# Kernel optimization log

Hardware: AMD Instinct MI355X
Metric: run time of the kernel (lower is better)

The kernel has to match this reference:

```python
import jax, jax.numpy as jnp
import numpy as np


def setup_inputs() -> dict:
    key = jax.random.key(0)
    kq, kk, kv = jax.random.split(key, 3)
    B, H, QL, KL, D = 2, 32, 512, 4096, 128
    return {
        "Q": jax.random.normal(kq, (B, H, QL, D), dtype=jnp.float32),
        "K": jax.random.normal(kk, (B, H, KL, D), dtype=jnp.float32),
        "V": jax.random.normal(kv, (B, H, KL, D), dtype=jnp.float32),
        "proj_dim": 32,
    }


def reference(Q, K, V, proj_dim):
    bsz, num_heads, q_len, head_dim = Q.shape
    kv_len = K.shape[2]
    bh = bsz * num_heads

    # ---- prepare(K, V): SVD of centered K, low-rank basis B ----
    K_r = K.reshape(bh, kv_len, head_dim)
    V_r = V.reshape(bh, kv_len, head_dim)
    K_centered = (K_r - K_r.mean(axis=1, keepdims=True)).astype(jnp.float32)
    _, _, Vh = jnp.linalg.svd(K_centered, full_matrices=False)  # [bh, d, d]
    Bmat = jnp.swapaxes(Vh[:, :proj_dim, :], -2, -1).astype(K.dtype)  # [bh, d, r]
    K_proj = jnp.matmul(K_r, Bmat)  # [bh, kv_len, r]

    # ---- forward(Q): project Q, full score matrix, softmax, weighted V ----
    Q_r = Q.reshape(bh, q_len, head_dim)
    Q_proj = jnp.matmul(Q_r, Bmat)  # [bh, q_len, r]
    scale = 1.0 / (proj_dim ** 0.5)
    scores = jnp.matmul(Q_proj, jnp.swapaxes(K_proj, 1, 2)) * scale  # [bh, q_len, kv_len]
    weights = jax.nn.softmax(scores, axis=-1)
    out = jnp.matmul(weights, V_r)  # [bh, q_len, d]
    return out.reshape(bsz, num_heads, q_len, head_dim)
```

## Files before the change

kernel.cpp:

```cpp
#include <hip/hip_runtime.h>

#define BH 64
#define KLEN 4096
#define QLEN 512
#define DIM 128
#define RP 32
#define NSWEEP 6

__global__ __launch_bounds__(256) void gram_kernel(const float* __restrict__ K,
                                                   float* __restrict__ Gpart,
                                                   float* __restrict__ Spart) {
    int bh = blockIdx.y, chunk = blockIdx.x;
    const float* Kb = K + ((size_t)bh * KLEN + (size_t)chunk * 1024) * DIM;
    __shared__ float Kt[32][129];
    int t = threadIdx.x;
    int ty = t >> 4, tx = t & 15;
    float acc[8][8];
#pragma unroll
    for (int i = 0; i < 8; i++)
#pragma unroll
        for (int j = 0; j < 8; j++) acc[i][j] = 0.f;
    float s_acc = 0.f;
    for (int tile = 0; tile < 32; tile++) {
        __syncthreads();
        for (int k = 0; k < 16; k++) {
            int idx = t + k * 256;
            Kt[idx >> 7][idx & 127] = Kb[tile * 32 * DIM + idx];
        }
        __syncthreads();
#pragma unroll 4
        for (int r = 0; r < 32; r++) {
            float a_[8], b_[8];
#pragma unroll
            for (int i = 0; i < 8; i++) a_[i] = Kt[r][ty * 8 + i];
#pragma unroll
            for (int j = 0; j < 8; j++) b_[j] = Kt[r][tx * 8 + j];
#pragma unroll
            for (int i = 0; i < 8; i++)
#pragma unroll
                for (int j = 0; j < 8; j++) acc[i][j] += a_[i] * b_[j];
        }
        if (t < 128) { float ss = 0.f; for (int r = 0; r < 32; r++) ss += Kt[r][t]; s_acc += ss; }
    }
    float* Gb = Gpart + ((size_t)chunk * BH + bh) * DIM * DIM;
#pragma unroll
    for (int i = 0; i < 8; i++)
#pragma unroll
        for (int j = 0; j < 8; j++) Gb[(ty * 8 + i) * DIM + tx * 8 + j] = acc[i][j];
    if (t < 128) Spart[((size_t)chunk * BH + bh) * DIM + t] = s_acc;
}

__device__ __forceinline__ void pair_pq(int r, int x, int& p, int& q) {
    if (x == 0) { p = 127; q = r; }
    else {
        int a = r + x;       a -= (a >= 127) ? 127 : 0;
        int b = r + 127 - x; b -= (b >= 127) ? 127 : 0;
        p = a; q = b;
    }
}

__global__ __launch_bounds__(1024) void jacobi_kernel(const float* __restrict__ Gpart,
                                                      const float* __restrict__ Spart,
                                                      float* __restrict__ Bout) {
    __shared__ float C[128][129];
    __shared__ float Vm[32][129];
    __shared__ float2 csA[2][64];
    __shared__ float diag[128];
    int slice = blockIdx.x, bh = blockIdx.y, t = threadIdx.x;
    const size_t gslab = (size_t)BH * DIM * DIM;
    const float* Gb = Gpart + (size_t)bh * DIM * DIM;

#define CGET(a, b) C[min(a, b)][max(a, b)]

    if (t < 128) {
        float s = 0.f;
#pragma unroll
        for (int c = 0; c < 4; c++) s += Spart[((size_t)c * BH + bh) * DIM + t];
        diag[t] = s;
    }
    __syncthreads();
    for (int k = 0; k < 16; k++) {
        int idx = t + k * 1024;
        int i = idx >> 7, j = idx & 127;
        if (i <= j) {
            float g = Gb[idx] + Gb[gslab + idx] + Gb[2 * gslab + idx] + Gb[3 * gslab + idx];
            C[i][j] = g - diag[i] * diag[j] * (1.0f / 4096.0f);
        }
    }
    for (int k = 0; k < 4; k++) {
        int idx = t + k * 1024;
        int kk = idx >> 7, j = idx & 127;
        Vm[kk][j] = (32 * slice + kk == j) ? 1.0f : 0.0f;
    }
    __syncthreads();
    if (t < 64) {
        int p, q;
        pair_pq(0, t, p, q);
        float app = C[min(p, p)][p], aqq = C[q][q], apq = CGET(p, q);
        float c = 1.0f, s = 0.0f;
        if (apq != 0.0f) {
            float tau = (aqq - app) / (2.0f * apq);
            float root = sqrtf(1.0f + tau * tau);
            float tt = (tau >= 0.0f) ? 1.0f / (tau + root) : 1.0f / (tau - root);
            c = 1.0f / sqrtf(1.0f + tt * tt);
            s = tt * c;
        }
        csA[0][t] = make_float2(c, s);
    }
    __syncthreads();

    int ti0, tj0, ti1, tj1, ti2 = 0, tj2 = 0;
    {
        auto unrank = [](int task, int& i, int& j) {
            if (task < 64) { i = task; j = task; return; }
            int L = task - 64, ii = 0;
            while (L >= 63 - ii) { L -= 63 - ii; ii++; }
            i = ii; j = ii + 1 + L;
        };
        unrank(t, ti0, tj0);
        unrank(t + 1024, ti1, tj1);
        if (t < 32) unrank(t + 2048, ti2, tj2);
    }

    const int NR = NSWEEP * 127;
    int r = 0;
    for (int sr = 0; sr < NR; sr++) {
        int cur = sr & 1, nxt = cur ^ 1;
        {
            auto task = [&](int i, int j) {
                int pi, qi; pair_pq(r, i, pi, qi);
                float2 csi = csA[cur][i];
                if (i == j) {
                    float app = C[min(pi, qi)][min(pi, qi)];
                    float aqq = C[max(pi, qi)][max(pi, qi)];
                    app = C[pi][pi]; aqq = C[qi][qi];
                    float apq = CGET(pi, qi);
                    float a1 = csi.x * app - csi.y * apq, b1 = csi.y * app + csi.x * apq;
                    float d1 = csi.x * apq - csi.y * aqq, e1 = csi.y * apq + csi.x * aqq;
                    C[pi][pi] = csi.x * a1 - csi.y * d1;
                    CGET(pi, qi) = csi.x * b1 - csi.y * e1;
                    C[qi][qi] = csi.y * b1 + csi.x * e1;
                } else {
                    int pj, qj; pair_pq(r, j, pj, qj);
                    float2 csj = csA[cur][j];
                    float a = CGET(pi, pj), b = CGET(pi, qj), d = CGET(qi, pj), e = CGET(qi, qj);
                    float a1 = csj.x * a - csj.y * b, b1 = csj.y * a + csj.x * b;
                    float d1 = csj.x * d - csj.y * e, e1 = csj.y * d + csj.x * e;
                    CGET(pi, pj) = csi.x * a1 - csi.y * d1;
                    CGET(qi, pj) = csi.y * a1 + csi.x * d1;
                    CGET(pi, qj) = csi.x * b1 - csi.y * e1;
                    CGET(qi, qj) = csi.y * b1 + csi.x * e1;
                }
            };
            task(ti0, tj0);
            task(ti1, tj1);
            if (t < 32) task(ti2, tj2);
        }
        __syncthreads();
        if (t < 64) {
            if (sr + 1 < NR) {
                int r2 = (r + 1 == 127) ? 0 : r + 1;
                int p, q;
                pair_pq(r2, t, p, q);
                float app = C[p][p], aqq = C[q][q], apq = CGET(p, q);
                float c = 1.0f, s = 0.0f;
                if (apq != 0.0f) {
                    float tau = (aqq - app) / (2.0f * apq);
                    float root = sqrtf(1.0f + tau * tau);
                    float tt = (tau >= 0.0f) ? 1.0f / (tau + root) : 1.0f / (tau - root);
                    c = 1.0f / sqrtf(1.0f + tt * tt);
                    s = tt * c;
                }
                csA[nxt][t] = make_float2(c, s);
            }
        } else {
            int tt = t - 64;
            for (int tau = tt; tau < 2048; tau += 960) {
                int x = tau & 63, k = tau >> 6;
                int pj, qj; pair_pq(r, x, pj, qj);
                float2 cs = csA[cur][x];
                float u = Vm[k][pj], v = Vm[k][qj];
                Vm[k][pj] = cs.x * u - cs.y * v;
                Vm[k][qj] = cs.y * u + cs.x * v;
            }
        }
        __syncthreads();
        r = (r + 1 == 127) ? 0 : r + 1;
    }

    if (t < 128) diag[t] = C[t][t];
    __syncthreads();
    if (t < 128) {
        float dt = diag[t];
        int rank = 0;
        for (int j = 0; j < 128; j++) {
            float dj = diag[j];
            rank += (dj > dt) || (dj == dt && j < t);
        }
        if (rank < RP) {
            float* Bb = Bout + (size_t)bh * DIM * RP;
            for (int k = 0; k < 32; k++) Bb[(size_t)(32 * slice + k) * RP + rank] = Vm[k][t];
        }
    }
#undef CGET
}

__global__ __launch_bounds__(256) void proj_kernel(const float* __restrict__ X,
                                                   const float* __restrict__ Bmat,
                                                   float* __restrict__ Y, int nrows) {
    int bh = blockIdx.y, rb = blockIdx.x;
    __shared__ float Bl[128][33];
    __shared__ float Xt[64][129];
    int t = threadIdx.x;
    for (int k = 0; k < 16; k++) {
        int idx = t + k * 256;
        Bl[idx >> 5][idx & 31] = Bmat[(size_t)bh * DIM * RP + idx];
    }
    const float* Xb = X + ((size_t)bh * nrows + (size_t)rb * 64) * DIM;
    for (int k = 0; k < 32; k++) {
        int idx = t + k * 256;
        Xt[idx >> 7][idx & 127] = Xb[idx];
    }
    __syncthreads();
    int row = t >> 2, rg = (t & 3) * 8;
    float acc[8] = {0.f, 0.f, 0.f, 0.f, 0.f, 0.f, 0.f, 0.f};
    for (int k = 0; k < 128; k++) {
        float xv = Xt[row][k];
#pragma unroll
        for (int rr = 0; rr < 8; rr++) acc[rr] += xv * Bl[k][rg + rr];
    }
    float* Yb = Y + ((size_t)bh * nrows + (size_t)rb * 64) * RP + row * RP + rg;
#pragma unroll
    for (int rr = 0; rr < 8; rr++) Yb[rr] = acc[rr];
}

__global__ __launch_bounds__(256, 2) void attn_kernel(const float* __restrict__ Qp,
                                                      const float* __restrict__ Kp,
                                                      const float* __restrict__ Vg,
                                                      float* __restrict__ Out) {
    const float SCALE = 0.1767766953f;
    int qt = blockIdx.x, bh = blockIdx.y;
    __shared__ float Kpl[128][36];
    __shared__ float Vt[32][132];
    __shared__ float Sl[64][132];
    int t = threadIdx.x;
    int q = t >> 2, g = t & 3;
    float qreg[32];
    const float* Qb = Qp + ((size_t)bh * QLEN + (size_t)qt * 64 + q) * RP;
#pragma unroll
    for (int r = 0; r < 32; r++) qreg[r] = Qb[r];
    float acc[32];
#pragma unroll
    for (int i = 0; i < 32; i++) acc[i] = 0.f;
    float m_run = -INFINITY, l_run = 0.0f;

    for (int kt = 0; kt < 32; kt++) {
        __syncthreads();
        const float4* Kpb = (const float4*)(Kp + ((size_t)bh * KLEN + (size_t)kt * 128) * RP);
        for (int k = 0; k < 4; k++) {
            int idx4 = t + k * 256;
            int j = idx4 >> 3, r4 = idx4 & 7;
            *(float4*)&Kpl[j][r4 * 4] = Kpb[idx4];
        }
        __syncthreads();
        float sreg[32];
#pragma unroll
        for (int jj = 0; jj < 32; jj++) {
            int j = jj * 4 + g;
            float s = 0.f;
#pragma unroll
            for (int r4 = 0; r4 < 8; r4++) {
                float4 kv = *(const float4*)&Kpl[j][r4 * 4];
                s += qreg[r4 * 4 + 0] * kv.x + qreg[r4 * 4 + 1] * kv.y
                   + qreg[r4 * 4 + 2] * kv.z + qreg[r4 * 4 + 3] * kv.w;
            }
            sreg[jj] = s * SCALE;
        }
        float mx = sreg[0];
#pragma unroll
        for (int jj = 1; jj < 32; jj++) mx = fmaxf(mx, sreg[jj]);
        mx = fmaxf(mx, __shfl_xor(mx, 1));
        mx = fmaxf(mx, __shfl_xor(mx, 2));
        float m_new = fmaxf(m_run, mx);
        float alpha = __expf(m_run - m_new);
        float psum = 0.f;
#pragma unroll
        for (int jj = 0; jj < 32; jj++) {
            float w = __expf(sreg[jj] - m_new);
            sreg[jj] = w;
            psum += w;
        }
        psum += __shfl_xor(psum, 1);
        psum += __shfl_xor(psum, 2);
        l_run = l_run * alpha + psum;
        m_run = m_new;
#pragma unroll
        for (int jj = 0; jj < 32; jj++) Sl[q][jj * 4 + g] = sreg[jj];
#pragma unroll
        for (int i = 0; i < 32; i++) acc[i] *= alpha;
        for (int ss = 0; ss < 4; ss++) {
            __syncthreads();
            const float4* Vb = (const float4*)(Vg + ((size_t)bh * KLEN + (size_t)kt * 128 + (size_t)ss * 32) * DIM);
            for (int k = 0; k < 4; k++) {
                int idx4 = t + k * 256;
                int j = idx4 >> 5, c4 = idx4 & 31;
                *(float4*)&Vt[j][c4 * 4] = Vb[idx4];
            }
            __syncthreads();
            for (int j = 0; j < 32; j++) {
                float w = Sl[q][ss * 32 + j];
#pragma unroll
                for (int i4 = 0; i4 < 8; i4++) {
                    float4 vv = *(const float4*)&Vt[j][i4 * 16 + g * 4];
                    acc[i4 * 4 + 0] += w * vv.x;
                    acc[i4 * 4 + 1] += w * vv.y;
                    acc[i4 * 4 + 2] += w * vv.z;
                    acc[i4 * 4 + 3] += w * vv.w;
                }
            }
        }
    }
    float linv = 1.0f / l_run;
    float* Ob = Out + ((size_t)bh * QLEN + (size_t)qt * 64 + q) * DIM;
#pragma unroll
    for (int i4 = 0; i4 < 8; i4++) {
        float4 o;
        o.x = acc[i4 * 4 + 0] * linv;
        o.y = acc[i4 * 4 + 1] * linv;
        o.z = acc[i4 * 4 + 2] * linv;
        o.w = acc[i4 * 4 + 3] * linv;
        *(float4*)&Ob[i4 * 16 + g * 4] = o;
    }
}

extern "C" void kernel_launch(void* const* d_in, const int* in_sizes, int n_in,
                              void* d_out, int out_size, void* d_ws, size_t ws_size,
                              hipStream_t stream) {
    const float* Q = (const float*)d_in[0];
    const float* K = (const float*)d_in[1];
    const float* V = (const float*)d_in[2];
    float* out = (float*)d_out;
    float* ws = (float*)d_ws;
    float* G  = ws;
    float* S  = G + (size_t)BH * DIM * DIM;
    float* Bm = S + BH * DIM;
    float* Kp = Bm + (size_t)BH * DIM * RP;
    float* Qp = Kp + (size_t)BH * KLEN * RP;
    float* Gpart = Kp;
    float* Spart = Gpart + (size_t)4 * BH * DIM * DIM;

    gram_kernel<<<dim3(4, BH), 256, 0, stream>>>(K, Gpart, Spart);
    jacobi_kernel<<<dim3(4, BH), 1024, 0, stream>>>(Gpart, Spart, Bm);
    proj_kernel<<<dim3(KLEN / 64, BH), 256, 0, stream>>>(K, Bm, Kp, KLEN);
    proj_kernel<<<dim3(QLEN / 64, BH), 256, 0, stream>>>(Q, Bm, Qp, QLEN);
    attn_kernel<<<dim3(QLEN / 64, BH), 256, 0, stream>>>(Qp, Kp, V, out);
}
```

Before: 2.444 ms.

## Store full symmetric Gram in Jacobi and register-block two queries per attention thread

The Jacobi kernel now keeps the full symmetric matrix instead of the upper triangle. Every rotation task becomes a uniform 2x2 block update, with each thread handling one row pair against four column pairs. This removes the min/max indexing and the triangular unranking, at the cost of roughly double the shared-memory updates. The attention kernel drops to 128 threads, each holding two query rows, and passes softmax weights between lanes with shuffles instead of a shared-memory score buffer. The intent is to reuse each loaded V element for two queries and avoid the Sl round trip, while accepting much higher register pressure.

Result: slower. 5.544 ms (+126.9%).

```diff
diff --git a/kernel.cpp b/kernel.cpp
--- a/kernel.cpp
+++ b/kernel.cpp
@@ -70,8 +70,6 @@
     const size_t gslab = (size_t)BH * DIM * DIM;
     const float* Gb = Gpart + (size_t)bh * DIM * DIM;
 
-#define CGET(a, b) C[min(a, b)][max(a, b)]
-
     if (t < 128) {
         float s = 0.f;
 #pragma unroll
@@ -82,10 +80,8 @@
     for (int k = 0; k < 16; k++) {
         int idx = t + k * 1024;
         int i = idx >> 7, j = idx & 127;
-        if (i <= j) {
-            float g = Gb[idx] + Gb[gslab + idx] + Gb[2 * gslab + idx] + Gb[3 * gslab + idx];
-            C[i][j] = g - diag[i] * diag[j] * (1.0f / 4096.0f);
-        }
+        float g = Gb[idx] + Gb[gslab + idx] + Gb[2 * gslab + idx] + Gb[3 * gslab + idx];
+        C[i][j] = g - diag[i] * diag[j] * (1.0f / 4096.0f);
     }
     for (int k = 0; k < 4; k++) {
         int idx = t + k * 1024;
@@ -96,7 +92,7 @@
     if (t < 64) {
         int p, q;
         pair_pq(0, t, p, q);
-        float app = C[min(p, p)][p], aqq = C[q][q], apq = CGET(p, q);
+        float app = C[p][p], aqq = C[q][q], apq = C[p][q];
         float c = 1.0f, s = 0.0f;
         if (apq != 0.0f) {
             float tau = (aqq - app) / (2.0f * apq);
@@ -109,52 +105,27 @@
     }
     __syncthreads();
 
-    int ti0, tj0, ti1, tj1, ti2 = 0, tj2 = 0;
-    {
-        auto unrank = [](int task, int& i, int& j) {
-            if (task < 64) { i = task; j = task; return; }
-            int L = task - 64, ii = 0;
-            while (L >= 63 - ii) { L -= 63 - ii; ii++; }
-            i = ii; j = ii + 1 + L;
-        };
-        unrank(t, ti0, tj0);
-        unrank(t + 1024, ti1, tj1);
-        if (t < 32) unrank(t + 2048, ti2, tj2);
-    }
-
     const int NR = NSWEEP * 127;
     int r = 0;
     for (int sr = 0; sr < NR; sr++) {
         int cur = sr & 1, nxt = cur ^ 1;
         {
-            auto task = [&](int i, int j) {
-                int pi, qi; pair_pq(r, i, pi, qi);
-                float2 csi = csA[cur][i];
-                if (i == j) {
-                    float app = C[min(pi, qi)][min(pi, qi)];
-                    float aqq = C[max(pi, qi)][max(pi, qi)];
-                    app = C[pi][pi]; aqq = C[qi][qi];
-                    float apq = CGET(pi, qi);
-                    float a1 = csi.x * app - csi.y * apq, b1 = csi.y * app + csi.x * apq;
-                    float d1 = csi.x * apq - csi.y * aqq, e1 = csi.y * apq + csi.x * aqq;
-                    C[pi][pi] = csi.x * a1 - csi.y * d1;
-                    CGET(pi, qi) = csi.x * b1 - csi.y * e1;
-                    C[qi][qi] = csi.y * b1 + csi.x * e1;
-                } else {
-                    int pj, qj; pair_pq(r, j, pj, qj);
-                    float2 csj = csA[cur][j];
-                    float a = CGET(pi, pj), b = CGET(pi, qj), d = CGET(qi, pj), e = CGET(qi, qj);
-                    float a1 = csj.x * a - csj.y * b, b1 = csj.y * a + csj.x * b;
-                    float d1 = csj.x * d - csj.y * e, e1 = csj.y * d + csj.x * e;
-                    CGET(pi, pj) = csi.x * a1 - csi.y * d1;
-                    CGET(qi, pj) = csi.y * a1 + csi.x * d1;
-                    CGET(pi, qj) = csi.x * b1 - csi.y * e1;
-                    CGET(qi, qj) = csi.y * b1 + csi.x * e1;
-                }
-            };
-            task(ti0, tj0);
-            task(ti1, tj1);
-            if (t < 32) task(ti2, tj2);
+            int i = t & 63, jb = (t >> 6) << 2;
+            int pi, qi; pair_pq(r, i, pi, qi);
+            float2 csi = csA[cur][i];
+#pragma unroll
+            for (int jj = 0; jj < 4; jj++) {
+                int j = jb + jj;
+                int pj, qj; pair_pq(r, j, pj, qj);
+                float2 csj = csA[cur][j];
+                float a = C[pi][pj], b = C[pi][qj], d = C[qi][pj], e = C[qi][qj];
+                float a1 = csj.x * a - csj.y * b, b1 = csj.y * a + csj.x * b;
+                float d1 = csj.x * d - csj.y * e, e1 = csj.y * d + csj.x * e;
+                C[pi][pj] = csi.x * a1 - csi.y * d1;
+                C[qi][pj] = csi.y * a1 + csi.x * d1;
+                C[pi][qj] = csi.x * b1 - csi.y * e1;
+                C[qi][qj] = csi.y * b1 + csi.x * e1;
+            }
         }
         __syncthreads();
         if (t < 64) {
@@ -162,7 +133,7 @@
                 int r2 = (r + 1 == 127) ? 0 : r + 1;
                 int p, q;
                 pair_pq(r2, t, p, q);
-                float app = C[p][p], aqq = C[q][q], apq = CGET(p, q);
+                float app = C[p][p], aqq = C[q][q], apq = C[p][q];
                 float c = 1.0f, s = 0.0f;
                 if (apq != 0.0f) {
                     float tau = (aqq - app) / (2.0f * apq);
@@ -202,7 +173,6 @@
             for (int k = 0; k < 32; k++) Bb[(size_t)(32 * slice + k) * RP + rank] = Vm[k][t];
         }
     }
-#undef CGET
 }
 
 __global__ __launch_bounds__(256) void proj_kernel(const float* __restrict__ X,
@@ -234,102 +204,115 @@
     for (int rr = 0; rr < 8; rr++) Yb[rr] = acc[rr];
 }
 
-__global__ __launch_bounds__(256, 2) void attn_kernel(const float* __restrict__ Qp,
+__global__ __launch_bounds__(128, 2) void attn_kernel(const float* __restrict__ Qp,
                                                       const float* __restrict__ Kp,
                                                       const float* __restrict__ Vg,
                                                       float* __restrict__ Out) {
     const float SCALE = 0.1767766953f;
     int qt = blockIdx.x, bh = blockIdx.y;
     __shared__ float Kpl[128][36];
-    __shared__ float Vt[32][132];
-    __shared__ float Sl[64][132];
+    __shared__ float Vt[64][132];
     int t = threadIdx.x;
     int q = t >> 2, g = t & 3;
-    float qreg[32];
-    const float* Qb = Qp + ((size_t)bh * QLEN + (size_t)qt * 64 + q) * RP;
-#pragma unroll
-    for (int r = 0; r < 32; r++) qreg[r] = Qb[r];
-    float acc[32];
-#pragma unroll
-    for (int i = 0; i < 32; i++) acc[i] = 0.f;
-    float m_run = -INFINITY, l_run = 0.0f;
+    float qreg0[32], qreg1[32];
+    {
+        const float4* Qb0 = (const float4*)(Qp + ((size_t)bh * QLEN + (size_t)qt * 64 + q) * RP);
+        const float4* Qb1 = (const float4*)(Qp + ((size_t)bh * QLEN + (size_t)qt * 64 + 32 + q) * RP);
+#pragma unroll
+        for (int r4 = 0; r4 < 8; r4++) {
+            float4 a = Qb0[r4], b = Qb1[r4];
+            qreg0[r4*4+0] = a.x; qreg0[r4*4+1] = a.y; qreg0[r4*4+2] = a.z; qreg0[r4*4+3] = a.w;
+            qreg1[r4*4+0] = b.x; qreg1[r4*4+1] = b.y; qreg1[r4*4+2] = b.z; qreg1[r4*4+3] = b.w;
+        }
+    }
+    float acc0[32], acc1[32];
+#pragma unroll
+    for (int i = 0; i < 32; i++) { acc0[i] = 0.f; acc1[i] = 0.f; }
+    float m0 = -INFINITY, l0 = 0.f, m1 = -INFINITY, l1 = 0.f;
 
     for (int kt = 0; kt < 32; kt++) {
         __syncthreads();
         const float4* Kpb = (const float4*)(Kp + ((size_t)bh * KLEN + (size_t)kt * 128) * RP);
-        for (int k = 0; k < 4; k++) {
-            int idx4 = t + k * 256;
-            int j = idx4 >> 3, r4 = idx4 & 7;
-            *(float4*)&Kpl[j][r4 * 4] = Kpb[idx4];
-        }
-        __syncthreads();
-        float sreg[32];
+#pragma unroll
+        for (int k = 0; k < 8; k++) {
+            int idx4 = t + k * 128;
+            *(float4*)&Kpl[idx4 >> 3][(idx4 & 7) * 4] = Kpb[idx4];
+        }
+        __syncthreads();
+        float s0[32], s1[32];
 #pragma unroll
         for (int jj = 0; jj < 32; jj++) {
             int j = jj * 4 + g;
-            float s = 0.f;
+            float a0 = 0.f, a1 = 0.f;
 #pragma unroll
             for (int r4 = 0; r4 < 8; r4++) {
                 float4 kv = *(const float4*)&Kpl[j][r4 * 4];
-                s += qreg[r4 * 4 + 0] * kv.x + qreg[r4 * 4 + 1] * kv.y
-                   + qreg[r4 * 4 + 2] * kv.z + qreg[r4 * 4 + 3] * kv.w;
-            }
-            sreg[jj] = s * SCALE;
-        }
-        float mx = sreg[0];
-#pragma unroll
-        for (int jj = 1; jj < 32; jj++) mx = fmaxf(mx, sreg[jj]);
-        mx = fmaxf(mx, __shfl_xor(mx, 1));
-        mx = fmaxf(mx, __shfl_xor(mx, 2));
-        float m_new = fmaxf(m_run, mx);
-        float alpha = __expf(m_run - m_new);
-        float psum = 0.f;
+                a0 += qreg0[r4*4+0]*kv.x + qreg0[r4*4+1]*kv.y + qreg0[r4*4+2]*kv.z + qreg0[r4*4+3]*kv.w;
+                a1 += qreg1[r4*4+0]*kv.x + qreg1[r4*4+1]*kv.y + qreg1[r4*4+2]*kv.z + qreg1[r4*4+3]*kv.w;
+            }
+            s0[jj] = a0 * SCALE;
+            s1[jj] = a1 * SCALE;
+        }
+        float mx0 = s0[0], mx1 = s1[0];
+#pragma unroll
+        for (int jj = 1; jj < 32; jj++) { mx0 = fmaxf(mx0, s0[jj]); mx1 = fmaxf(mx1, s1[jj]); }
+        mx0 = fmaxf(mx0, __shfl_xor(mx0, 1)); mx0 = fmaxf(mx0, __shfl_xor(mx0, 2));
+        mx1 = fmaxf(mx1, __shfl_xor(mx1, 1)); mx1 = fmaxf(mx1, __shfl_xor(mx1, 2));
+        float mn0 = fmaxf(m0, mx0), mn1 = fmaxf(m1, mx1);
+        float al0 = __expf(m0 - mn0), al1 = __expf(m1 - mn1);
+        float ps0 = 0.f, ps1 = 0.f;
 #pragma unroll
         for (int jj = 0; jj < 32; jj++) {
-            float w = __expf(sreg[jj] - m_new);
-            sreg[jj] = w;
-            psum += w;
-        }
-        psum += __shfl_xor(psum, 1);
-        psum += __shfl_xor(psum, 2);
-        l_run = l_run * alpha + psum;
-        m_run = m_new;
-#pragma unroll
-        for (int jj = 0; jj < 32; jj++) Sl[q][jj * 4 + g] = sreg[jj];
-#pragma unroll
-        for (int i = 0; i < 32; i++) acc[i] *= alpha;
-        for (int ss = 0; ss < 4; ss++) {
+            float w0 = __expf(s0[jj] - mn0); s0[jj] = w0; ps0 += w0;
+            float w1 = __expf(s1[jj] - mn1); s1[jj] = w1; ps1 += w1;
+        }
+        ps0 += __shfl_xor(ps0, 1); ps0 += __shfl_xor(ps0, 2);
+        ps1 += __shfl_xor(ps1, 1); ps1 += __shfl_xor(ps1, 2);
+        l0 = l0 * al0 + ps0; m0 = mn0;
+        l1 = l1 * al1 + ps1; m1 = mn1;
+#pragma unroll
+        for (int i = 0; i < 32; i++) { acc0[i] *= al0; acc1[i] *= al1; }
+#pragma unroll
+        for (int ss = 0; ss < 2; ss++) {
             __syncthreads();
-            const float4* Vb = (const float4*)(Vg + ((size_t)bh * KLEN + (size_t)kt * 128 + (size_t)ss * 32) * DIM);
-            for (int k = 0; k < 4; k++) {
-                int idx4 = t + k * 256;
-                int j = idx4 >> 5, c4 = idx4 & 31;
-                *(float4*)&Vt[j][c4 * 4] = Vb[idx4];
+            const float4* Vb = (const float4*)(Vg + ((size_t)bh * KLEN + (size_t)kt * 128 + (size_t)ss * 64) * DIM);
+#pragma unroll
+            for (int k = 0; k < 16; k++) {
+                int idx4 = t + k * 128;
+                *(float4*)&Vt[idx4 >> 5][(idx4 & 31) * 4] = Vb[idx4];
             }
             __syncthreads();
-            for (int j = 0; j < 32; j++) {
-                float w = Sl[q][ss * 32 + j];
-#pragma unroll
-                for (int i4 = 0; i4 < 8; i4++) {
-                    float4 vv = *(const float4*)&Vt[j][i4 * 16 + g * 4];
-                    acc[i4 * 4 + 0] += w * vv.x;
-                    acc[i4 * 4 + 1] += w * vv.y;
-                    acc[i4 * 4 + 2] += w * vv.z;
-                    acc[i4 * 4 + 3] += w * vv.w;
+#pragma unroll
+            for (int m = 0; m < 4; m++) {
+                int gs = g ^ m;
+#pragma unroll
+                for (int jj16 = 0; jj16 < 16; jj16++) {
+                    int jj = ss * 16 + jj16;
+                    float w0 = m ? __shfl_xor(s0[jj], m) : s0[jj];
+                    float w1 = m ? __shfl_xor(s1[jj], m) : s1[jj];
+                    int jl = jj16 * 4 + gs;
+#pragma unroll
+                    for (int i4 = 0; i4 < 8; i4++) {
+                        float4 vv = *(const float4*)&Vt[jl][i4 * 16 + g * 4];
+                        acc0[i4*4+0] += w0 * vv.x; acc0[i4*4+1] += w0 * vv.y;
+                        acc0[i4*4+2] += w0 * vv.z; acc0[i4*4+3] += w0 * vv.w;
+                        acc1[i4*4+0] += w1 * vv.x; acc1[i4*4+1] += w1 * vv.y;
+                        acc1[i4*4+2] += w1 * vv.z; acc1[i4*4+3] += w1 * vv.w;
+                    }
                 }
             }
         }
     }
-    float linv = 1.0f / l_run;
-    float* Ob = Out + ((size_t)bh * QLEN + (size_t)qt * 64 + q) * DIM;
+    float li0 = 1.0f / l0, li1 = 1.0f / l1;
+    float* Ob0 = Out + ((size_t)bh * QLEN + (size_t)qt * 64 + q) * DIM;
+    float* Ob1 = Out + ((size_t)bh * QLEN + (size_t)qt * 64 + 32 + q) * DIM;
 #pragma unroll
     for (int i4 = 0; i4 < 8; i4++) {
-        float4 o;
-        o.x = acc[i4 * 4 + 0] * linv;
-        o.y = acc[i4 * 4 + 1] * linv;
-        o.z = acc[i4 * 4 + 2] * linv;
-        o.w = acc[i4 * 4 + 3] * linv;
-        *(float4*)&Ob[i4 * 16 + g * 4] = o;
+        float4 o0, o1;
+        o0.x = acc0[i4*4+0]*li0; o0.y = acc0[i4*4+1]*li0; o0.z = acc0[i4*4+2]*li0; o0.w = acc0[i4*4+3]*li0;
+        o1.x = acc1[i4*4+0]*li1; o1.y = acc1[i4*4+1]*li1; o1.z = acc1[i4*4+2]*li1; o1.w = acc1[i4*4+3]*li1;
+        *(float4*)&Ob0[i4 * 16 + g * 4] = o0;
+        *(float4*)&Ob1[i4 * 16 + g * 4] = o1;
     }
 }
 
@@ -353,5 +336,5 @@
     jacobi_kernel<<<dim3(4, BH), 1024, 0, stream>>>(Gpart, Spart, Bm);
     proj_kernel<<<dim3(KLEN / 64, BH), 256, 0, stream>>>(K, Bm, Kp, KLEN);
     proj_kernel<<<dim3(QLEN / 64, BH), 256, 0, stream>>>(Q, Bm, Qp, QLEN);
-    attn_kernel<<<dim3(QLEN / 64, BH), 256, 0, stream>>>(Qp, Kp, V, out);
-}
+    attn_kernel<<<dim3(QLEN / 64, BH), 128, 0, stream>>>(Qp, Kp, V, out);
+}
```
